# Kernel tuning notes

Hardware: AMD Instinct MI355X
Metric: run time of the kernel (lower is better)

Reference implementation:

```python
import jax, jax.numpy as jnp
import numpy as np
import math

B, H, S, D = 8, 16, 256, 256  # S == D is required by the module's math

def setup_inputs() -> dict:
    key = jax.random.key(0)
    kq, kk, kv, km = jax.random.split(key, 4)
    q = jax.random.normal(kq, (B, H, S, D), dtype=jnp.float32)
    k = jax.random.normal(kk, (B, H, S, D), dtype=jnp.float32)
    v = jax.random.normal(kv, (B, H, S, D), dtype=jnp.float32)
    u = jax.random.uniform(km, (1, H, S, S), dtype=jnp.float32)
    # additive mask: large negative where 'masked', 0.0 elsewhere
    mask = jnp.where(u > 0.7, jnp.float32(-1000.0), jnp.float32(0.0))
    return {"q": q, "k": k, "v": v, "mask": mask}

def reference(q, k, v, mask):
    scale = 1.0 / math.sqrt(q.shape[-1])
    # qk: [B,H,S,S]
    qk = jnp.einsum('bhsd,bhtd->bhst', q, k) * scale + mask
    # first matmul with v: [B,H,S,D] (D == S)
    attn = jnp.einsum('bhst,bhtd->bhsd', qk, v)
    # masked_fill where additive mask == 0.0 (broadcasts [1,H,S,S] -> [B,H,S,D])
    attn = jnp.where(mask == 0.0, jnp.float32(-1e9), attn)
    attn = jax.nn.softmax(attn.astype(jnp.float32), axis=-1).astype(q.dtype)
    # second matmul with v: [B,H,S,D]
    out = jnp.einsum('bhst,bhtd->bhsd', attn, v)
    return out
```

## Files before the change

### kernel.cpp

```cpp
#include <hip/hip_runtime.h>
#include <math.h>

namespace {
constexpr int S  = 256;
constexpr int NT = 256;
constexpr float SCALE = 0.0625f;
constexpr int KLD = 264;
}

typedef _Float16 f16x4 __attribute__((ext_vector_type(4)));
typedef _Float16 f16x8 __attribute__((ext_vector_type(8)));
typedef float    f32x4 __attribute__((ext_vector_type(4)));

#define MFMA(a, b, c) __builtin_amdgcn_mfma_f32_16x16x32_f16((a), (b), (c), 0, 0, 0)

__global__ __launch_bounds__(NT, 2) void prep_kernel(
    const float* __restrict__ q, const float* __restrict__ k,
    const float* __restrict__ v,
    _Float16* __restrict__ vth, _Float16* __restrict__ vtl,
    _Float16* __restrict__ r_hi, _Float16* __restrict__ r_lo,
    int nbh, int swzq)
{
    __shared__ __align__(16) unsigned char lds_arena[64 * KLD * 2 * 2];

    const int tid  = threadIdx.x;
    const int trio = blockIdx.x / 3;
    const int role = blockIdx.x % 3;

    if (role < 2) {
        _Float16* kh = (_Float16*)lds_arena;
        _Float16* kl = kh + 64 * KLD;

        const int w = tid >> 6, l = tid & 63, l15 = l & 15, l4 = l >> 4;

        int L = trio * 2 + role;
        if (swzq) {
            const int n = nbh * 16;
            L = (L & 7) * (n >> 3) + (L >> 3);
        }
        const int bh = L >> 4;
        const int s0 = ((L >> 2) & 3) << 6;
        const int t0 = (L & 3) << 6;

        const float* qb = q + ((size_t)bh << 16);
        const float* kb = k + ((size_t)bh << 16);

        {
            const float* ksrc = kb + (size_t)t0 * S;
            float4 kf[16];
            #pragma unroll
            for (int it = 0; it < 16; ++it)
                kf[it] = *(const float4*)&ksrc[it * 1024 + tid * 4];
            #pragma unroll
            for (int it = 0; it < 16; ++it) {
                const int idx = it * 1024 + tid * 4;
                const float xs[4] = {kf[it].x, kf[it].y, kf[it].z, kf[it].w};
                f16x4 hv, lv;
                #pragma unroll
                for (int e = 0; e < 4; ++e) {
                    const _Float16 hi = (_Float16)xs[e];
                    hv[e] = hi; lv[e] = (_Float16)(xs[e] - (float)hi);
                }
                const int row = idx >> 8;
                const int col = idx & 255;
                *(f16x4*)&kh[row * KLD + col] = hv;
                *(f16x4*)&kl[row * KLD + col] = lv;
            }
        }

        f16x8 qh[8], ql[8];
        {
            const float* qr = qb + (size_t)(s0 + 16 * w + l15) * S;
            float4 qf[16];
            #pragma unroll
            for (int kc = 0; kc < 8; ++kc) {
                qf[2 * kc]     = *(const float4*)&qr[kc * 32 + l4 * 8];
                qf[2 * kc + 1] = *(const float4*)&qr[kc * 32 + l4 * 8 + 4];
            }
            #pragma unroll
            for (int kc = 0; kc < 8; ++kc) {
                const float xs[8] = {qf[2*kc].x, qf[2*kc].y, qf[2*kc].z, qf[2*kc].w,
                                     qf[2*kc+1].x, qf[2*kc+1].y, qf[2*kc+1].z, qf[2*kc+1].w};
                f16x8 hv, lv;
                #pragma unroll
                for (int e = 0; e < 8; ++e) {
                    const float x = xs[e] * SCALE;
                    const _Float16 hi = (_Float16)x;
                    hv[e] = hi; lv[e] = (_Float16)(x - (float)hi);
                }
                qh[kc] = hv; ql[kc] = lv;
            }
        }
        __syncthreads();

        f32x4 acc[4];
        #pragma unroll
        for (int j = 0; j < 4; ++j) acc[j] = (f32x4){0.f, 0.f, 0.f, 0.f};

        #pragma unroll
        for (int kc = 0; kc < 8; ++kc) {
            #pragma unroll
            for (int j = 0; j < 4; ++j) {
                const int bo = (j * 16 + l15) * KLD + kc * 32 + l4 * 8;
                const f16x8 khf = *(const f16x8*)&kh[bo];
                const f16x8 klf = *(const f16x8*)&kl[bo];
                acc[j] = MFMA(qh[kc], khf, acc[j]);
                acc[j] = MFMA(qh[kc], klf, acc[j]);
                acc[j] = MFMA(ql[kc], khf, acc[j]);
            }
        }
        __syncthreads();

        _Float16* rb = kh + w * 2048;
        #pragma unroll
        for (int j = 0; j < 4; ++j) {
            const int tcgl = j >> 1;
            const int jj   = j & 1;
            #pragma unroll
            for (int rr = 0; rr < 4; ++rr) {
                const float rv = acc[j][rr];
                const _Float16 hi = (_Float16)rv;
                const _Float16 lo = (_Float16)(rv - (float)hi);
                const int elem = ((l4 * 4 + rr) + 16 * (2 * jj + (l15 >> 3))) * 8
                               + (l15 & 7);
                rb[tcgl * 1024 + elem]       = hi;
                rb[tcgl * 1024 + 512 + elem] = lo;
            }
        }
        const int sb = (s0 >> 4) + w;
        const size_t hb = (size_t)bh << 16;
        #pragma unroll
        for (int tcgl = 0; tcgl < 2; ++tcgl) {
            const f16x8 ph = *(const f16x8*)&rb[tcgl * 1024 + l * 8];
            const f16x8 pl = *(const f16x8*)&rb[tcgl * 1024 + 512 + l * 8];
            const size_t oi = hb + (size_t)sb * 4096
                            + (size_t)((t0 >> 5) + tcgl) * 512 + l * 8;
            *(f16x8*)&r_hi[oi] = ph;
            *(f16x8*)&r_lo[oi] = pl;
        }
    } else {
        float (*tile)[257] = (float(*)[257])lds_arena;

        const int vi = trio;
        const int bh = vi >> 3;
        const int tc = vi & 7;

        const float* vb = v + (size_t)bh * S * S + (size_t)tc * 32 * S;
        {
            const int c4 = (tid & 63) * 4;
            const int r  = tid >> 6;
            float4 vf[8];
            #pragma unroll
            for (int rr = 0; rr < 8; ++rr)
                vf[rr] = *(const float4*)&vb[(size_t)(rr * 4 + r) * S + c4];
            #pragma unroll
            for (int rr = 0; rr < 8; ++rr) {
                const int row = rr * 4 + r;
                tile[row][c4 + 0] = vf[rr].x; tile[row][c4 + 1] = vf[rr].y;
                tile[row][c4 + 2] = vf[rr].z; tile[row][c4 + 3] = vf[rr].w;
            }
        }
        __syncthreads();

        const size_t obase = (size_t)bh * S * S + (size_t)tc * 8192;
        #pragma unroll
        for (int it = 0; it < 4; ++it) {
            const int id  = it * 256 + tid;
            const int j   = id >> 6;
            const int l4  = (id >> 4) & 3;
            const int l15 = id & 15;
            const int d   = j * 16 + l15;
            const int t0  = l4 * 8;
            f16x8 hv, lv;
            #pragma unroll
            for (int e = 0; e < 8; ++e) {
                const float x = tile[t0 + e][d];
                const _Float16 hi = (_Float16)x;
                hv[e] = hi; lv[e] = (_Float16)(x - (float)hi);
            }
            const size_t oi = obase + (size_t)id * 8;
            *(f16x8*)&vth[oi] = hv;
            *(f16x8*)&vtl[oi] = lv;
        }
    }
}

#define SRC_OF(sp) ((sp) == 0 ? vth : vtl)

#define P2_LOAD(tc)                                                           \
    _Pragma("unroll")                                                         \
    for (int r_ = 0; r_ < 8; ++r_) {                                          \
        const int sp_ = r_ >> 2, qt_ = r_ & 3;                                \
        const _Float16* s_ = SRC_OF(sp_);                                     \
        stg[r_] = *(const f16x8*)&s_[hb + (size_t)(tc) * 8192 + qt_ * 2048 + tid * 8]; \
    }

#define P2_WRITE()                                                            \
    _Pragma("unroll")                                                         \
    for (int r_ = 0; r_ < 8; ++r_) {                                          \
        const int sp_ = r_ >> 2, qt_ = r_ & 3;                                \
        *(f16x8*)&arena[sp_ * 8192 + qt_ * 2048 + tid * 8] = stg[r_];         \
    }

#define P3_LOAD(tc)                                                           \
    _Pragma("unroll")                                                         \
    for (int r_ = 0; r_ < 8; ++r_) {                                          \
        const int sp_ = r_ >> 2, qt_ = r_ & 3;                                \
        const _Float16* s_ = SRC_OF(sp_);                                     \
        stg[r_] = *(const f16x8*)&s_[hb + (size_t)(tc) * 8192 + qt_ * 2048 + tid * 8]; \
    }

#define P3_WRITE()                                                            \
    _Pragma("unroll")                                                         \
    for (int r_ = 0; r_ < 8; ++r_) {                                          \
        const int sp_ = r_ >> 2, qt_ = r_ & 3;                                \
        *(f16x8*)&arena[16384 + sp_ * 8192 + qt_ * 2048 + tid * 8] = stg[r_]; \
    }

__global__ __launch_bounds__(NT, 2) void attn2_kernel(
    const float* __restrict__ mask,
    const _Float16* __restrict__ r_hi, const _Float16* __restrict__ r_lo,
    const _Float16* __restrict__ vth, const _Float16* __restrict__ vtl,
    float* __restrict__ out, int H, int swz)
{
    __shared__ __align__(16) _Float16 arena[32768];

    const int tid = threadIdx.x;
    const int w = tid >> 6, l = tid & 63, l15 = l & 15, l4 = l >> 4;

    int L = blockIdx.x;
    if (swz) L = (blockIdx.x & 7) * ((int)gridDim.x >> 3) + (blockIdx.x >> 3);
    const int bh = L >> 2;
    const int s0 = (L & 3) << 6;
    const int h  = bh % H;

    const size_t hb = (size_t)bh << 16;
    const float* mbase = mask + ((size_t)h << 16);

    const int sb_a = (s0 >> 4) + w;
    const _Float16* rh_p = r_hi + hb + (size_t)sb_a * 4096;
    const _Float16* rl_p = r_lo + hb + (size_t)sb_a * 4096;
    const float*    m_p  = mbase + (size_t)(s0 + 16 * w + l15) * S;

    f16x8 stg[8];

    f32x4 acc2[16];
    #pragma unroll
    for (int j = 0; j < 16; ++j) acc2[j] = (f32x4){0.f, 0.f, 0.f, 0.f};

    P2_LOAD(0);
    P2_WRITE();
    P2_LOAD(1);
    f16x8 rhc, rlc; float4 m0c, m1c;
    {
        rhc = *(const f16x8*)&rh_p[l * 8];
        rlc = *(const f16x8*)&rl_p[l * 8];
        m0c = *(const float4*)&m_p[l4 * 8];
        m1c = *(const float4*)&m_p[l4 * 8 + 4];
    }
    __syncthreads();

    #pragma unroll
    for (int tc = 0; tc < 8; ++tc) {
        f16x8 rhn, rln; float4 m0n, m1n;
        if (tc < 7) {
            rhn = *(const f16x8*)&rh_p[(tc + 1) * 512 + l * 8];
            rln = *(const f16x8*)&rl_p[(tc + 1) * 512 + l * 8];
            const int ko_ = (tc + 1) * 32 + l4 * 8;
            m0n = *(const float4*)&m_p[ko_];
            m1n = *(const float4*)&m_p[ko_ + 4];
        }
        f16x8 mf;
        mf[0] = (_Float16)m0c.x; mf[1] = (_Float16)m0c.y;
        mf[2] = (_Float16)m0c.z; mf[3] = (_Float16)m0c.w;
        mf[4] = (_Float16)m1c.x; mf[5] = (_Float16)m1c.y;
        mf[6] = (_Float16)m1c.z; mf[7] = (_Float16)m1c.w;

        __builtin_amdgcn_s_setprio(1);
        #pragma unroll
        for (int j = 0; j < 16; ++j) {
            const int fo = j * 512 + l * 8;
            const f16x8 vh = *(const f16x8*)&arena[fo];
            const f16x8 vl = *(const f16x8*)&arena[8192 + fo];
            acc2[j] = MFMA(mf,  vh, acc2[j]);
            acc2[j] = MFMA(mf,  vl, acc2[j]);
            acc2[j] = MFMA(rhc, vh, acc2[j]);
            acc2[j] = MFMA(rhc, vl, acc2[j]);
            acc2[j] = MFMA(rlc, vh, acc2[j]);
        }
        __builtin_amdgcn_s_setprio(0);
        __syncthreads();
        if (tc < 7) {
            P2_WRITE();
            if (tc < 6) P2_LOAD(tc + 2);
            rhc = rhn; rlc = rln; m0c = m0n; m1c = m1n;
            __syncthreads();
        }
    }

    P3_LOAD(0);

    #pragma unroll
    for (int rr = 0; rr < 4; ++rr) {
        const int srow = 16 * w + l4 * 4 + rr;
        const float* mrow = mbase + (size_t)(s0 + srow) * S;
        float mx = -3.4e38f;
        #pragma unroll
        for (int j = 0; j < 16; ++j) {
            const float mval = mrow[j * 16 + l15];
            const float a = (mval == 0.0f) ? -1e9f : acc2[j][rr];
            acc2[j][rr] = a;
            mx = fmaxf(mx, a);
        }
        #pragma unroll
        for (int off = 1; off < 16; off <<= 1)
            mx = fmaxf(mx, __shfl_xor(mx, off, 64));
        float sm = 0.f;
        #pragma unroll
        for (int j = 0; j < 16; ++j) {
            const float e = __expf(acc2[j][rr] - mx);
            acc2[j][rr] = e;
            sm += e;
        }
        #pragma unroll
        for (int off = 1; off < 16; off <<= 1)
            sm += __shfl_xor(sm, off, 64);
        const float inv = 1.0f / sm;
        #pragma unroll
        for (int j = 0; j < 16; ++j) {
            const int t = j * 16 + l15;
            arena[((srow << 8) + t) ^ ((srow & 7) << 3)] = (_Float16)(acc2[j][rr] * inv);
        }
    }
    P3_WRITE();
    P3_LOAD(1);
    __syncthreads();

    f32x4 acc3[16];
    #pragma unroll
    for (int j = 0; j < 16; ++j) acc3[j] = (f32x4){0.f, 0.f, 0.f, 0.f};

    const int prow = 16 * w + l15;
    #pragma unroll
    for (int tc = 0; tc < 8; ++tc) {
        const int pb = ((prow << 8) + tc * 32 + l4 * 8) ^ ((prow & 7) << 3);
        const f16x8 pa = *(const f16x8*)&arena[pb];
        __builtin_amdgcn_s_setprio(1);
        #pragma unroll
        for (int j = 0; j < 16; ++j) {
            const int fo = 16384 + j * 512 + l * 8;
            acc3[j] = MFMA(pa, *(const f16x8*)&arena[fo], acc3[j]);
            acc3[j] = MFMA(pa, *(const f16x8*)&arena[8192 + fo], acc3[j]);
        }
        __builtin_amdgcn_s_setprio(0);
        __syncthreads();
        if (tc < 7) {
            P3_WRITE();
            if (tc < 6) P3_LOAD(tc + 2);
            __syncthreads();
        }
    }

    float* ob = out + hb + (size_t)s0 * S;
    #pragma unroll
    for (int j = 0; j < 16; ++j) {
        #pragma unroll
        for (int rr = 0; rr < 4; ++rr)
            ob[(size_t)(16 * w + l4 * 4 + rr) * S + j * 16 + l15] = acc3[j][rr];
    }
}

__global__ __launch_bounds__(NT) void transpose_k_kernel(
    const float* __restrict__ k, float* __restrict__ kt)
{
    __shared__ float tile[64][65];
    const int tileIdx = blockIdx.x & 15;
    const int bh      = blockIdx.x >> 4;
    const int ti = (tileIdx >> 2) * 64;
    const int tj = (tileIdx & 3) * 64;
    const float* kb = k  + (size_t)bh * S * S;
    float*      ktb = kt + (size_t)bh * S * S;
    const int c  = threadIdx.x & 63;
    const int r4 = threadIdx.x >> 6;
    #pragma unroll
    for (int rr = 0; rr < 64; rr += 4)
        tile[rr + r4][c] = kb[(size_t)(ti + rr + r4) * S + tj + c];
    __syncthreads();
    #pragma unroll
    for (int rr = 0; rr < 64; rr += 4)
        ktb[(size_t)(tj + rr + r4) * S + ti + c] = tile[c][rr + r4];
}

template <int RPB>
__global__ __launch_bounds__(NT) void fused_attn_rpb(
    const float* __restrict__ q, const float* __restrict__ kt,
    const float* __restrict__ v, const float* __restrict__ mask,
    float* __restrict__ out, int nbh, int H, int swizzle)
{
    __shared__ float qT[S][RPB];
    __shared__ float sT[S][RPB];
    __shared__ float redbuf[4][RPB];

    const int tid = threadIdx.x;
    constexpr int NRB = S / RPB;
    int bh, rb;
    if (swizzle) {
        const int xcd  = blockIdx.x & 7;
        const int slot = blockIdx.x >> 3;
        const int hpx  = nbh >> 3;
        bh = xcd * hpx + (slot % hpx);
        rb = slot / hpx;
    } else {
        bh = blockIdx.x / NRB;
        rb = blockIdx.x % NRB;
    }
    const int h  = bh % H;
    const int s0 = rb * RPB;

    const float* qb  = q    + (size_t)bh * S * S;
    const float* ktb = kt   + (size_t)bh * S * S;
    const float* vb  = v    + (size_t)bh * S * S;
    const float* mb  = mask + (size_t)h  * S * S + (size_t)s0 * S;
    float*       ob  = out  + (size_t)bh * S * S + (size_t)s0 * S;

    #pragma unroll
    for (int si = 0; si < RPB; ++si)
        qT[tid][si] = qb[(size_t)(s0 + si) * S + tid];
    __syncthreads();

    {
        float acc[RPB];
        #pragma unroll
        for (int si = 0; si < RPB; ++si) acc[si] = 0.f;
        #pragma unroll 4
        for (int i = 0; i < S; ++i) {
            const float kv = ktb[(size_t)i * S + tid];
            #pragma unroll
            for (int si4 = 0; si4 < RPB; si4 += 4) {
                const float4 qa = *reinterpret_cast<const float4*>(&qT[i][si4]);
                acc[si4+0] = fmaf(qa.x, kv, acc[si4+0]);
                acc[si4+1] = fmaf(qa.y, kv, acc[si4+1]);
                acc[si4+2] = fmaf(qa.z, kv, acc[si4+2]);
                acc[si4+3] = fmaf(qa.w, kv, acc[si4+3]);
            }
        }
        #pragma unroll
        for (int si4 = 0; si4 < RPB; si4 += 4) {
            float4 t4;
            t4.x = fmaf(acc[si4+0], SCALE, mb[(size_t)(si4+0)*S + tid]);
            t4.y = fmaf(acc[si4+1], SCALE, mb[(size_t)(si4+1)*S + tid]);
            t4.z = fmaf(acc[si4+2], SCALE, mb[(size_t)(si4+2)*S + tid]);
            t4.w = fmaf(acc[si4+3], SCALE, mb[(size_t)(si4+3)*S + tid]);
            *reinterpret_cast<float4*>(&sT[tid][si4]) = t4;
        }
    }
    __syncthreads();

    float a1[RPB];
    #pragma unroll
    for (int si = 0; si < RPB; ++si) a1[si] = 0.f;
    #pragma unroll 2
    for (int t = 0; t < S; ++t) {
        const float vv = vb[(size_t)t * S + tid];
        #pragma unroll
        for (int si4 = 0; si4 < RPB; si4 += 4) {
            const float4 pa = *reinterpret_cast<const float4*>(&sT[t][si4]);
            a1[si4+0] = fmaf(pa.x, vv, a1[si4+0]);
            a1[si4+1] = fmaf(pa.y, vv, a1[si4+1]);
            a1[si4+2] = fmaf(pa.z, vv, a1[si4+2]);
            a1[si4+3] = fmaf(pa.w, vv, a1[si4+3]);
        }
    }
    #pragma unroll
    for (int si = 0; si < RPB; ++si)
        if (mb[(size_t)si * S + tid] == 0.0f) a1[si] = -1e9f;

    const int lane = tid & 63;
    const int wv   = tid >> 6;
    #pragma unroll
    for (int si = 0; si < RPB; ++si) {
        float m = a1[si];
        #pragma unroll
        for (int off = 32; off > 0; off >>= 1)
            m = fmaxf(m, __shfl_down(m, off, 64));
        if (lane == 0) redbuf[wv][si] = m;
    }
    __syncthreads();
    float e[RPB];
    #pragma unroll
    for (int si = 0; si < RPB; ++si) {
        const float m = fmaxf(fmaxf(redbuf[0][si], redbuf[1][si]),
                              fmaxf(redbuf[2][si], redbuf[3][si]));
        e[si] = __expf(a1[si] - m);
    }
    __syncthreads();
    #pragma unroll
    for (int si = 0; si < RPB; ++si) {
        float sm = e[si];
        #pragma unroll
        for (int off = 32; off > 0; off >>= 1)
            sm += __shfl_down(sm, off, 64);
        if (lane == 0) redbuf[wv][si] = sm;
    }
    __syncthreads();
    #pragma unroll
    for (int si4 = 0; si4 < RPB; si4 += 4) {
        float4 t4;
        #pragma unroll
        for (int jj = 0; jj < 4; ++jj) {
            const int si = si4 + jj;
            const float sm = redbuf[0][si] + redbuf[1][si] +
                             redbuf[2][si] + redbuf[3][si];
            (&t4.x)[jj] = e[si] / sm;
        }
        *reinterpret_cast<float4*>(&sT[tid][si4]) = t4;
    }
    __syncthreads();

    float o[RPB];
    #pragma unroll
    for (int si = 0; si < RPB; ++si) o[si] = 0.f;
    #pragma unroll 2
    for (int t = 0; t < S; ++t) {
        const float vv = vb[(size_t)t * S + tid];
        #pragma unroll
        for (int si4 = 0; si4 < RPB; si4 += 4) {
            const float4 pa = *reinterpret_cast<const float4*>(&sT[t][si4]);
            o[si4+0] = fmaf(pa.x, vv, o[si4+0]);
            o[si4+1] = fmaf(pa.y, vv, o[si4+1]);
            o[si4+2] = fmaf(pa.z, vv, o[si4+2]);
            o[si4+3] = fmaf(pa.w, vv, o[si4+3]);
        }
    }
    #pragma unroll
    for (int si = 0; si < RPB; ++si)
        ob[(size_t)si * S + tid] = o[si];
}

extern "C" void kernel_launch(void* const* d_in, const int* in_sizes, int n_in,
                              void* d_out, int out_size, void* d_ws, size_t ws_size,
                              hipStream_t stream) {
    const float* q    = (const float*)d_in[0];
    const float* k    = (const float*)d_in[1];
    const float* v    = (const float*)d_in[2];
    const float* mask = (const float*)d_in[3];
    float* out = (float*)d_out;

    const int nbh = in_sizes[0] / (S * S);
    const int H   = in_sizes[3] / (S * S);
    const size_t he = (size_t)nbh * S * S;
    const size_t need = he * sizeof(_Float16) * 4;
    const size_t kt_bytes = he * sizeof(float);

    if (ws_size >= need) {
        _Float16* vth = (_Float16*)d_ws;
        _Float16* vtl = vth + he;
        _Float16* rhi = vtl + he;
        _Float16* rlo = rhi + he;
        const int nblk_q = nbh * 16;
        const int nblk_a = nbh * 4;
        const int swzq = (nblk_q % 8 == 0) ? 1 : 0;
        const int swza = (nblk_a % 8 == 0) ? 1 : 0;
        prep_kernel<<<dim3(nbh * 24), NT, 0, stream>>>(
            q, k, v, vth, vtl, rhi, rlo, nbh, swzq);
        attn2_kernel<<<dim3(nblk_a), NT, 0, stream>>>(
            mask, rhi, rlo, vth, vtl, out, H, swza);
    } else if (ws_size >= kt_bytes) {
        float* kt = (float*)d_ws;
        transpose_k_kernel<<<dim3(nbh * 16), NT, 0, stream>>>(k, kt);
        constexpr int RPB = 16;
        const int grid = nbh * (S / RPB);
        const int swz = (nbh % 8 == 0) ? 1 : 0;
        fused_attn_rpb<RPB><<<dim3(grid), NT, 0, stream>>>(
            q, kt, v, mask, out, nbh, H, swz);
    }
}
```

Baseline: 78.86 us.

## Split K tile staging into two halves to halve LDS and raise occupancy

The prep kernel now stages the 64-row K tile through LDS in two 32-row halves instead of all at once, halving the shared-memory arena. The second half's global loads are issued before the first half's MFMA loop so they overlap compute, and launch bounds are raised from 2 to 4 blocks per CU. This trades extra barriers and tighter register budgets, which risk spills, for higher occupancy and load/compute overlap.

```diff
diff --git a/kernel.cpp b/kernel.cpp
--- a/kernel.cpp
+++ b/kernel.cpp
@@ -14,14 +14,14 @@
 
 #define MFMA(a, b, c) __builtin_amdgcn_mfma_f32_16x16x32_f16((a), (b), (c), 0, 0, 0)
 
-__global__ __launch_bounds__(NT, 2) void prep_kernel(
+__global__ __launch_bounds__(NT, 4) void prep_kernel(
     const float* __restrict__ q, const float* __restrict__ k,
     const float* __restrict__ v,
     _Float16* __restrict__ vth, _Float16* __restrict__ vtl,
     _Float16* __restrict__ r_hi, _Float16* __restrict__ r_lo,
     int nbh, int swzq)
 {
-    __shared__ __align__(16) unsigned char lds_arena[64 * KLD * 2 * 2];
+    __shared__ __align__(16) unsigned char lds_arena[32 * KLD * 2 * 2];
 
     const int tid  = threadIdx.x;
     const int trio = blockIdx.x / 3;
@@ -29,7 +29,7 @@
 
     if (role < 2) {
         _Float16* kh = (_Float16*)lds_arena;
-        _Float16* kl = kh + 64 * KLD;
+        _Float16* kl = kh + 32 * KLD;
 
         const int w = tid >> 6, l = tid & 63, l15 = l & 15, l4 = l >> 4;
 
@@ -44,29 +44,12 @@
 
         const float* qb = q + ((size_t)bh << 16);
         const float* kb = k + ((size_t)bh << 16);
-
-        {
-            const float* ksrc = kb + (size_t)t0 * S;
-            float4 kf[16];
-            #pragma unroll
-            for (int it = 0; it < 16; ++it)
-                kf[it] = *(const float4*)&ksrc[it * 1024 + tid * 4];
-            #pragma unroll
-            for (int it = 0; it < 16; ++it) {
-                const int idx = it * 1024 + tid * 4;
-                const float xs[4] = {kf[it].x, kf[it].y, kf[it].z, kf[it].w};
-                f16x4 hv, lv;
-                #pragma unroll
-                for (int e = 0; e < 4; ++e) {
-                    const _Float16 hi = (_Float16)xs[e];
-                    hv[e] = hi; lv[e] = (_Float16)(xs[e] - (float)hi);
-                }
-                const int row = idx >> 8;
-                const int col = idx & 255;
-                *(f16x4*)&kh[row * KLD + col] = hv;
-                *(f16x4*)&kl[row * KLD + col] = lv;
-            }
-        }
+        const float* ksrc = kb + (size_t)t0 * S;
+
+        float4 kf0[8];
+        #pragma unroll
+        for (int it = 0; it < 8; ++it)
+            kf0[it] = *(const float4*)&ksrc[it * 1024 + tid * 4];
 
         f16x8 qh[8], ql[8];
         {
@@ -91,6 +74,26 @@
                 qh[kc] = hv; ql[kc] = lv;
             }
         }
+
+        #pragma unroll
+        for (int it = 0; it < 8; ++it) {
+            const int idx = it * 1024 + tid * 4;
+            const float xs[4] = {kf0[it].x, kf0[it].y, kf0[it].z, kf0[it].w};
+            f16x4 hv, lv;
+            #pragma unroll
+            for (int e = 0; e < 4; ++e) {
+                const _Float16 hi = (_Float16)xs[e];
+                hv[e] = hi; lv[e] = (_Float16)(xs[e] - (float)hi);
+            }
+            const int row = idx >> 8;
+            const int col = idx & 255;
+            *(f16x4*)&kh[row * KLD + col] = hv;
+            *(f16x4*)&kl[row * KLD + col] = lv;
+        }
+        float4 kf1[8];
+        #pragma unroll
+        for (int it = 0; it < 8; ++it)
+            kf1[it] = *(const float4*)&ksrc[8192 + it * 1024 + tid * 4];
         __syncthreads();
 
         f32x4 acc[4];
@@ -100,13 +103,44 @@
         #pragma unroll
         for (int kc = 0; kc < 8; ++kc) {
             #pragma unroll
-            for (int j = 0; j < 4; ++j) {
-                const int bo = (j * 16 + l15) * KLD + kc * 32 + l4 * 8;
+            for (int jl = 0; jl < 2; ++jl) {
+                const int bo = (jl * 16 + l15) * KLD + kc * 32 + l4 * 8;
                 const f16x8 khf = *(const f16x8*)&kh[bo];
                 const f16x8 klf = *(const f16x8*)&kl[bo];
-                acc[j] = MFMA(qh[kc], khf, acc[j]);
-                acc[j] = MFMA(qh[kc], klf, acc[j]);
-                acc[j] = MFMA(ql[kc], khf, acc[j]);
+                acc[jl] = MFMA(qh[kc], khf, acc[jl]);
+                acc[jl] = MFMA(qh[kc], klf, acc[jl]);
+                acc[jl] = MFMA(ql[kc], khf, acc[jl]);
+            }
+        }
+        __syncthreads();
+
+        #pragma unroll
+        for (int it = 0; it < 8; ++it) {
+            const int idx = it * 1024 + tid * 4;
+            const float xs[4] = {kf1[it].x, kf1[it].y, kf1[it].z, kf1[it].w};
+            f16x4 hv, lv;
+            #pragma unroll
+            for (int e = 0; e < 4; ++e) {
+                const _Float16 hi = (_Float16)xs[e];
+                hv[e] = hi; lv[e] = (_Float16)(xs[e] - (float)hi);
+            }
+            const int row = idx >> 8;
+            const int col = idx & 255;
+            *(f16x4*)&kh[row * KLD + col] = hv;
+            *(f16x4*)&kl[row * KLD + col] = lv;
+        }
+        __syncthreads();
+
+        #pragma unroll
+        for (int kc = 0; kc < 8; ++kc) {
+            #pragma unroll
+            for (int jl = 0; jl < 2; ++jl) {
+                const int bo = (jl * 16 + l15) * KLD + kc * 32 + l4 * 8;
+                const f16x8 khf = *(const f16x8*)&kh[bo];
+                const f16x8 klf = *(const f16x8*)&kl[bo];
+                acc[2 + jl] = MFMA(qh[kc], khf, acc[2 + jl]);
+                acc[2 + jl] = MFMA(qh[kc], klf, acc[2 + jl]);
+                acc[2 + jl] = MFMA(ql[kc], khf, acc[2 + jl]);
             }
         }
         __syncthreads();
```

After: 81.50 us. 1.03x slower.
